# Kernel tuning notes

Hardware: AMD Instinct MI355X
Metric: run time of the kernel (lower is better)

The kernel has to match this reference:

```python
import jax, jax.numpy as jnp
import numpy as np

L = 6
LN_EPS = 1e-5

def _ln(x):
    # LayerNorm over last dim, no affine (matches nn.LayerNorm(D, elementwise_affine=False))
    m = jnp.mean(x, axis=-1, keepdims=True)
    v = jnp.var(x, axis=-1, keepdims=True)
    return (x - m) / jnp.sqrt(v + LN_EPS)

def setup_inputs() -> dict:
    key = jax.random.key(0)
    ks = jax.random.split(key, 6)
    B, S, N, D, V = 2, 2048, 4096, 1024, 32000
    return {
        "input_": jax.random.randint(ks[0], (B, S), 0, V),
        "emb": jax.random.normal(ks[1], (V, D), jnp.float32) * 0.02,
        "Dx": jax.random.normal(ks[2], (D, N), jnp.float32) * 0.02,
        "Dy": jax.random.normal(ks[3], (D, N), jnp.float32) * 0.02,
        "E": jax.random.normal(ks[4], (N, D), jnp.float32) * 0.02,
        "readout": jax.random.normal(ks[5], (D, V), jnp.float32) * 0.02,
    }

def reference(input_, emb, Dx, Dy, E, readout):
    v_ast = emb[input_]  # [B,S,D]
    for _ in range(L):
        x = jax.nn.relu(jnp.einsum('bsd,dn->bsn', v_ast, Dx))  # [B,S,N]
        # linear attention Q@K.mT@V reassociated: x @ (x.mT @ v)
        kv = jnp.einsum('bsn,bsd->bnd', x, v_ast)              # [B,N,D]
        a_ast = jnp.einsum('bsn,bnd->bsd', x, kv)              # [B,S,D]
        y = jax.nn.relu(jnp.einsum('bsd,dn->bsn', a_ast, Dy)) * x  # [B,S,N]
        v_ast = _ln(v_ast + _ln(jnp.einsum('bsn,nd->bsd', y, E)))
    return jnp.einsum('bsd,dv->bsv', v_ast, readout)  # [B,S,vocab]
```

## Files before the change

### kernel.cpp

```cpp
#include <hip/hip_runtime.h>
#include <stdint.h>

typedef unsigned short u16;
typedef __bf16 bf16x8 __attribute__((ext_vector_type(8)));
typedef float  floatx4 __attribute__((ext_vector_type(4)));
typedef u16    ushort4v __attribute__((ext_vector_type(4)));
typedef u16    ushort8v __attribute__((ext_vector_type(8)));

#define B_ 2
#define S_ 2048
#define D_ 1024
#define N_ 4096
#define V_ 32000
#define R_ (B_ * S_)
#define L_ 6

__device__ __forceinline__ u16 f2bf(float f) {
  union { float f; uint32_t u; } v; v.f = f;
  uint32_t r = v.u + 0x7fffu + ((v.u >> 16) & 1u);
  return (u16)(r >> 16);
}
__device__ __forceinline__ float bf2f(u16 h) {
  union { uint32_t u; float f; } v; v.u = ((uint32_t)h) << 16;
  return v.f;
}

#define LDSW 40

template<int MODE>
__global__ __launch_bounds__(256)
void gemm_bt(const u16* __restrict__ A, const u16* __restrict__ BT,
             void* __restrict__ Cv, const u16* __restrict__ Mul,
             int M, int N, int K, size_t sA, size_t sBT, size_t sC)
{
  __shared__ __align__(16) u16 As[128 * LDSW];
  __shared__ __align__(16) u16 Bs[128 * LDSW];

  const int tid  = threadIdx.x;
  const int lane = tid & 63;
  const int wave = tid >> 6;
  const int r = lane & 15;
  const int q = lane >> 4;
  const int wm = (wave >> 1) << 6;
  const int wn = (wave & 1) << 6;
  const long m0 = (long)blockIdx.y * 128;
  const long n0 = (long)blockIdx.x * 128;

  const u16* Ab = A  + (size_t)blockIdx.z * sA;
  const u16* Bb = BT + (size_t)blockIdx.z * sBT;

  const int srow = tid >> 2;
  const int scol = (tid & 3) << 3;
  const u16* a_src = Ab + (size_t)(m0 + srow) * K + scol;
  const u16* b_src = Bb + (size_t)(n0 + srow) * K + scol;
  u16* a_dst = &As[srow * LDSW + scol];
  u16* b_dst = &Bs[srow * LDSW + scol];

  const floatx4 zero = {0.f, 0.f, 0.f, 0.f};
  floatx4 acc[4][4];
#pragma unroll
  for (int i = 0; i < 4; ++i)
#pragma unroll
    for (int j = 0; j < 4; ++j) acc[i][j] = zero;

  for (int kt = 0; kt < K; kt += 32) {
    __syncthreads();
    *(ushort8v*)a_dst              = *(const ushort8v*)(a_src + kt);
    *(ushort8v*)(a_dst + 64*LDSW)  = *(const ushort8v*)(a_src + (size_t)64 * K + kt);
    *(ushort8v*)b_dst              = *(const ushort8v*)(b_src + kt);
    *(ushort8v*)(b_dst + 64*LDSW)  = *(const ushort8v*)(b_src + (size_t)64 * K + kt);
    __syncthreads();

    bf16x8 af[4], bfr[4];
#pragma unroll
    for (int i = 0; i < 4; ++i)
      af[i]  = *(const bf16x8*)&As[(wm + i*16 + r) * LDSW + (q << 3)];
#pragma unroll
    for (int j = 0; j < 4; ++j)
      bfr[j] = *(const bf16x8*)&Bs[(wn + j*16 + r) * LDSW + (q << 3)];
#pragma unroll
    for (int i = 0; i < 4; ++i)
#pragma unroll
      for (int j = 0; j < 4; ++j)
        acc[i][j] = __builtin_amdgcn_mfma_f32_16x16x32_bf16(af[i], bfr[j], acc[i][j], 0, 0, 0);
  }

  const long crow0 = m0 + wm + (q << 2);
  const long ccol0 = n0 + wn + r;
#pragma unroll
  for (int i = 0; i < 4; ++i) {
#pragma unroll
    for (int j = 0; j < 4; ++j) {
      const long col = ccol0 + j * 16;
#pragma unroll
      for (int ii = 0; ii < 4; ++ii) {
        const long row = crow0 + i * 16 + ii;
        float v = acc[i][j][ii];
        if (MODE == 1 || MODE == 2) v = fmaxf(v, 0.f);
        const size_t off = (size_t)row * N + col;
        if (MODE == 2) v *= bf2f(Mul[off]);
        if (MODE == 3) (((float*)Cv) + (size_t)blockIdx.z * sC)[off] = v;
        else           (((u16*)Cv)   + (size_t)blockIdx.z * sC)[off] = f2bf(v);
      }
    }
  }
}

__global__ __launch_bounds__(256)
void transpose_bf16(const u16* __restrict__ src, u16* __restrict__ dst, int R, int C)
{
  __shared__ __align__(16) u16 tile[64][68];
  const int t = threadIdx.x;
  const long r0 = (long)blockIdx.y * 64;
  const long c0 = (long)blockIdx.x * 64;
  const int tc = (t & 15) << 2;
  const int tr = t >> 4;
#pragma unroll
  for (int i = 0; i < 4; ++i) {
    const int rr = tr + (i << 4);
    *(ushort4v*)&tile[rr][tc] = *(const ushort4v*)(src + (size_t)(r0 + rr) * C + c0 + tc);
  }
  __syncthreads();
#pragma unroll
  for (int i = 0; i < 4; ++i) {
    const int cc = tr + (i << 4);
    ushort4v v;
#pragma unroll
    for (int j = 0; j < 4; ++j) v[j] = tile[tc + j][cc];
    *(ushort4v*)(dst + (size_t)(c0 + cc) * R + r0 + tc) = v;
  }
}

__global__ __launch_bounds__(256)
void cvt_transpose(const float* __restrict__ src, u16* __restrict__ dst, int R, int C)
{
  __shared__ __align__(16) u16 tile[64][68];
  const int t = threadIdx.x;
  const long r0 = (long)blockIdx.y * 64;
  const long c0 = (long)blockIdx.x * 64;
  const int tc = (t & 15) << 2;
  const int tr = t >> 4;
#pragma unroll
  for (int i = 0; i < 4; ++i) {
    const int rr = tr + (i << 4);
    const float4 v = *(const float4*)(src + (size_t)(r0 + rr) * C + c0 + tc);
    ushort4v h = {f2bf(v.x), f2bf(v.y), f2bf(v.z), f2bf(v.w)};
    *(ushort4v*)&tile[rr][tc] = h;
  }
  __syncthreads();
#pragma unroll
  for (int i = 0; i < 4; ++i) {
    const int cc = tr + (i << 4);
    ushort4v v;
#pragma unroll
    for (int j = 0; j < 4; ++j) v[j] = tile[tc + j][cc];
    *(ushort4v*)(dst + (size_t)(c0 + cc) * R + r0 + tc) = v;
  }
}

__global__ __launch_bounds__(256)
void embed_k(const int* __restrict__ idx, const float* __restrict__ emb,
             float* __restrict__ vf, u16* __restrict__ vb)
{
  const size_t row = blockIdx.x;
  const int t = threadIdx.x;
  const int id = idx[row];
  const float4 x = ((const float4*)(emb + (size_t)id * D_))[t];
  ((float4*)(vf + row * D_))[t] = x;
  ushort4v h = {f2bf(x.x), f2bf(x.y), f2bf(x.z), f2bf(x.w)};
  ((ushort4v*)(vb + row * D_))[t] = h;
}

__device__ __forceinline__ float block_sum(float v, float* red, int t) {
#pragma unroll
  for (int o = 32; o > 0; o >>= 1) v += __shfl_down(v, o, 64);
  __syncthreads();
  if ((t & 63) == 0) red[t >> 6] = v;
  __syncthreads();
  return red[0] + red[1] + red[2] + red[3];
}

__global__ __launch_bounds__(256)
void ln_k(const float* __restrict__ z, float* __restrict__ vf, u16* __restrict__ vb)
{
  __shared__ float red[4];
  const int t = threadIdx.x;
  const size_t row = blockIdx.x;
  const float4 zv = ((const float4*)(z + row * D_))[t];
  float s = zv.x + zv.y + zv.z + zv.w;
  const float mean = block_sum(s, red, t) * (1.0f / D_);
  float4 d;
  d.x = zv.x - mean; d.y = zv.y - mean; d.z = zv.z - mean; d.w = zv.w - mean;
  float s2 = d.x*d.x + d.y*d.y + d.z*d.z + d.w*d.w;
  const float var = block_sum(s2, red, t) * (1.0f / D_);
  const float inv = rsqrtf(var + 1e-5f);
  const float4 vv = ((const float4*)(vf + row * D_))[t];
  float4 w;
  w.x = vv.x + d.x * inv; w.y = vv.y + d.y * inv;
  w.z = vv.z + d.z * inv; w.w = vv.w + d.w * inv;
  float sw = w.x + w.y + w.z + w.w;
  const float mean2 = block_sum(sw, red, t) * (1.0f / D_);
  float4 d2;
  d2.x = w.x - mean2; d2.y = w.y - mean2; d2.z = w.z - mean2; d2.w = w.w - mean2;
  float s22 = d2.x*d2.x + d2.y*d2.y + d2.z*d2.z + d2.w*d2.w;
  const float var2 = block_sum(s22, red, t) * (1.0f / D_);
  const float inv2 = rsqrtf(var2 + 1e-5f);
  float4 o;
  o.x = d2.x * inv2; o.y = d2.y * inv2; o.z = d2.z * inv2; o.w = d2.w * inv2;
  ((float4*)(vf + row * D_))[t] = o;
  ushort4v h = {f2bf(o.x), f2bf(o.y), f2bf(o.z), f2bf(o.w)};
  ((ushort4v*)(vb + row * D_))[t] = h;
}

extern "C" void kernel_launch(void* const* d_in, const int* in_sizes, int n_in,
                              void* d_out, int out_size, void* d_ws, size_t ws_size,
                              hipStream_t stream)
{
  const int*   inp = (const int*)d_in[0];
  const float* emb = (const float*)d_in[1];
  const float* Dx  = (const float*)d_in[2];
  const float* Dy  = (const float*)d_in[3];
  const float* E   = (const float*)d_in[4];
  const float* ro  = (const float*)d_in[5];
  float* out = (float*)d_out;

  char* p = (char*)d_ws;
  auto take = [&](size_t n) { char* q = p; p += (n + 255) & ~(size_t)255; return q; };
  float* vf  = (float*)take((size_t)R_ * D_ * 4);
  float* zf  = (float*)take((size_t)R_ * D_ * 4);
  u16* vb    = (u16*)take((size_t)R_ * D_ * 2);
  u16* vbT   = (u16*)take((size_t)R_ * D_ * 2);
  u16* xb    = (u16*)take((size_t)R_ * N_ * 2);
  u16* xbT   = (u16*)take((size_t)R_ * N_ * 2);
  u16* yb    = (u16*)take((size_t)R_ * N_ * 2);
  u16* kvT   = (u16*)take((size_t)B_ * D_ * N_ * 2);
  u16* ab    = (u16*)take((size_t)R_ * D_ * 2);
  u16* DxT   = (u16*)take((size_t)D_ * N_ * 2);
  u16* DyT   = (u16*)take((size_t)D_ * N_ * 2);
  u16* ET    = (u16*)take((size_t)D_ * N_ * 2);
  u16* roT   = (u16*)take((size_t)D_ * V_ * 2);

  const dim3 blk(256);

  cvt_transpose<<<dim3(N_/64, D_/64), blk, 0, stream>>>(Dx, DxT, D_, N_);
  cvt_transpose<<<dim3(N_/64, D_/64), blk, 0, stream>>>(Dy, DyT, D_, N_);
  cvt_transpose<<<dim3(D_/64, N_/64), blk, 0, stream>>>(E,  ET,  N_, D_);
  cvt_transpose<<<dim3(V_/64, D_/64), blk, 0, stream>>>(ro, roT, D_, V_);

  embed_k<<<dim3(R_), blk, 0, stream>>>(inp, emb, vf, vb);
  for (int b = 0; b < B_; ++b)
    transpose_bf16<<<dim3(D_/64, S_/64), blk, 0, stream>>>(
        vb + (size_t)b*S_*D_, vbT + (size_t)b*D_*S_, S_, D_);

  for (int l = 0; l < L_; ++l) {
    gemm_bt<1><<<dim3(N_/128, R_/128, 1), blk, 0, stream>>>(
        vb, DxT, xb, nullptr, R_, N_, D_, 0, 0, 0);
    for (int b = 0; b < B_; ++b)
      transpose_bf16<<<dim3(N_/64, S_/64), blk, 0, stream>>>(
          xb + (size_t)b*S_*N_, xbT + (size_t)b*N_*S_, S_, N_);
    gemm_bt<0><<<dim3(N_/128, D_/128, B_), blk, 0, stream>>>(
        vbT, xbT, kvT, nullptr, D_, N_, S_,
        (size_t)D_*S_, (size_t)N_*S_, (size_t)D_*N_);
    gemm_bt<0><<<dim3(D_/128, S_/128, B_), blk, 0, stream>>>(
        xb, kvT, ab, nullptr, S_, D_, N_,
        (size_t)S_*N_, (size_t)D_*N_, (size_t)S_*D_);
    gemm_bt<2><<<dim3(N_/128, R_/128, 1), blk, 0, stream>>>(
        ab, DyT, yb, xb, R_, N_, D_, 0, 0, 0);
    gemm_bt<3><<<dim3(D_/128, R_/128, 1), blk, 0, stream>>>(
        yb, ET, zf, nullptr, R_, D_, N_, 0, 0, 0);
    ln_k<<<dim3(R_), blk, 0, stream>>>(zf, vf, vb);
    for (int b = 0; b < B_; ++b)
      transpose_bf16<<<dim3(D_/64, S_/64), blk, 0, stream>>>(
          vb + (size_t)b*S_*D_, vbT + (size_t)b*D_*S_, S_, D_);
  }

  gemm_bt<3><<<dim3(V_/128, R_/128, 1), blk, 0, stream>>>(
      vb, roT, out, nullptr, R_, V_, D_, 0, 0, 0);
}
```

Before: 3.481 ms.

## Load GEMM tiles directly into LDS and remap block order for cache reuse

```diff
diff --git a/kernel.cpp b/kernel.cpp
--- a/kernel.cpp
+++ b/kernel.cpp
@@ -25,7 +25,11 @@
   return v.f;
 }
 
-#define LDSW 40
+__device__ __forceinline__ void gload16(const u16* g, u16* l) {
+  auto* gp = (__attribute__((address_space(1))) void*)const_cast<u16*>(g);
+  auto* lp = (__attribute__((address_space(3))) void*)l;
+  __builtin_amdgcn_global_load_lds(gp, lp, 16, 0, 0);
+}
 
 template<int MODE>
 __global__ __launch_bounds__(256)
@@ -33,8 +37,8 @@
              void* __restrict__ Cv, const u16* __restrict__ Mul,
              int M, int N, int K, size_t sA, size_t sBT, size_t sC)
 {
-  __shared__ __align__(16) u16 As[128 * LDSW];
-  __shared__ __align__(16) u16 Bs[128 * LDSW];
+  __shared__ __align__(16) u16 As[128 * 32];
+  __shared__ __align__(16) u16 Bs[128 * 32];
 
   const int tid  = threadIdx.x;
   const int lane = tid & 63;
@@ -43,18 +47,27 @@
   const int q = lane >> 4;
   const int wm = (wave >> 1) << 6;
   const int wn = (wave & 1) << 6;
-  const long m0 = (long)blockIdx.y * 128;
-  const long n0 = (long)blockIdx.x * 128;
+
+  const int nby = gridDim.y;
+  const int bid = blockIdx.y * gridDim.x + blockIdx.x;
+  const int bx  = bid / nby;
+  const int by  = bid - bx * nby;
+  const long m0 = (long)by * 128;
+  const long n0 = (long)bx * 128;
 
   const u16* Ab = A  + (size_t)blockIdx.z * sA;
   const u16* Bb = BT + (size_t)blockIdx.z * sBT;
 
   const int srow = tid >> 2;
   const int scol = (tid & 3) << 3;
-  const u16* a_src = Ab + (size_t)(m0 + srow) * K + scol;
-  const u16* b_src = Bb + (size_t)(n0 + srow) * K + scol;
-  u16* a_dst = &As[srow * LDSW + scol];
-  u16* b_dst = &Bs[srow * LDSW + scol];
+  const u16* a_src0 = Ab + (size_t)(m0 + srow) * K + scol;
+  const u16* a_src1 = a_src0 + (size_t)64 * K;
+  const u16* b_src0 = Bb + (size_t)(n0 + srow) * K + scol;
+  const u16* b_src1 = b_src0 + (size_t)64 * K;
+  u16* a_d0 = &As[wave * 512];
+  u16* a_d1 = &As[2048 + wave * 512];
+  u16* b_d0 = &Bs[wave * 512];
+  u16* b_d1 = &Bs[2048 + wave * 512];
 
   const floatx4 zero = {0.f, 0.f, 0.f, 0.f};
   floatx4 acc[4][4];
@@ -65,19 +78,19 @@
 
   for (int kt = 0; kt < K; kt += 32) {
     __syncthreads();
-    *(ushort8v*)a_dst              = *(const ushort8v*)(a_src + kt);
-    *(ushort8v*)(a_dst + 64*LDSW)  = *(const ushort8v*)(a_src + (size_t)64 * K + kt);
-    *(ushort8v*)b_dst              = *(const ushort8v*)(b_src + kt);
-    *(ushort8v*)(b_dst + 64*LDSW)  = *(const ushort8v*)(b_src + (size_t)64 * K + kt);
+    gload16(a_src0 + kt, a_d0);
+    gload16(a_src1 + kt, a_d1);
+    gload16(b_src0 + kt, b_d0);
+    gload16(b_src1 + kt, b_d1);
     __syncthreads();
 
     bf16x8 af[4], bfr[4];
 #pragma unroll
     for (int i = 0; i < 4; ++i)
-      af[i]  = *(const bf16x8*)&As[(wm + i*16 + r) * LDSW + (q << 3)];
+      af[i]  = *(const bf16x8*)&As[(wm + i*16 + r) * 32 + (q << 3)];
 #pragma unroll
     for (int j = 0; j < 4; ++j)
-      bfr[j] = *(const bf16x8*)&Bs[(wn + j*16 + r) * LDSW + (q << 3)];
+      bfr[j] = *(const bf16x8*)&Bs[(wn + j*16 + r) * 32 + (q << 3)];
 #pragma unroll
     for (int i = 0; i < 4; ++i)
 #pragma unroll
```

Measured after the change: 3.350 ms. 3.8% less time.
